# Optimization experiments

Measured on AMD Instinct MI355X. Metric: run time of the kernel, lower is better.

The kernel has to match this reference:

```python
import jax, jax.numpy as jnp
import numpy as np

B, C, D = 16384, 512, 512
EXT = 2
H = C * EXT
TAU = 1.0          # temperature_train
STEP = 0.05        # langevin_step_size
NOISE = 0.1        # langevin_noise
STEPS = 32         # langevin_steps


def setup_inputs() -> dict:
    key = jax.random.key(0)
    ks = jax.random.split(key, 8)
    s_in = 1.0 / np.sqrt(D)
    s_h = 1.0 / np.sqrt(H)
    return {
        'x': jax.random.normal(ks[0], (B, D), jnp.float32),
        'vanilla_components': jnp.abs(jax.random.normal(ks[1], (C, D), jnp.float32) * 0.1),
        'e_sp': jax.random.normal(ks[2], (C * D,), jnp.float32) * 0.1,
        'W1e': jax.random.normal(ks[3], (D, H), jnp.float32) * s_in,
        'b1e': jnp.zeros((H,), jnp.float32),
        'W2e': jax.random.normal(ks[4], (H, C), jnp.float32) * s_h,
        'b2e': jnp.zeros((C,), jnp.float32),
        'W1r': jax.random.normal(ks[5], (D, H), jnp.float32) * s_in,
        'b1r': jnp.zeros((H,), jnp.float32),
        'W2r': jax.random.normal(ks[6], (H, C), jnp.float32) * s_h,
        'b2r': jnp.zeros((C,), jnp.float32),
    }


def _langevin_gate(e, key):
    """Langevin MCMC on latent u with quadratic energy E(u)=0.5||u||^2 + <e,u>.
    Returns selection probability sigmoid(-u/tau)."""
    def step(u, k):
        grad = u + e  # dE/du
        u = u - STEP * grad + NOISE * jax.random.normal(k, u.shape, u.dtype)
        return u, None
    u, _ = jax.lax.scan(step, jnp.zeros_like(e), jax.random.split(key, STEPS))
    return jax.nn.sigmoid(-u / TAU)


def reference(x, vanilla_components, e_sp, W1e, b1e, W2e, b2e, W1r, b1r, W2r, b2r):
    k1, k2 = jax.random.split(jax.random.key(42))
    # non-negative components
    comps = jnp.abs(vanilla_components)  # [C, D]
    # fixed energy-based sparsity mask over component entries
    p_sp = _langevin_gate(e_sp, k1).reshape(C, D)
    comps = comps * p_sp
    # dynamic per-sample component selection energies via MLP
    h = jax.nn.relu(x @ W1e + b1e)          # [B, H]
    e_dyn = h @ W2e + b2e                   # [B, C]
    gate = _langevin_gate(e_dyn, k2)        # [B, C] soft gates (train mode)
    hr = jax.nn.relu(x @ W1r + b1r)         # [B, H]
    conc = (hr @ W2r + b2r) * gate          # [B, C]
    # aggregate: (concentration * components).sum over components -> [B, D]
    return conc @ comps
```

## Files before the change

### kernel.cpp

```cpp
#include <hip/hip_runtime.h>
#include <hip/hip_bf16.h>
#include <stdint.h>

#define Bn 16384
#define Cn 512
#define Dn 512
#define Hn 1024

#define A32 0.80628851f

typedef __attribute__((ext_vector_type(8))) short bf16x8;
typedef __attribute__((ext_vector_type(4))) float f32x4;
typedef __attribute__((ext_vector_type(2))) float f32x2;

__device__ __forceinline__ ushort f2bf(float f) {
  uint32_t u = __float_as_uint(f);
  return (ushort)((u + 0x7fffu + ((u >> 16) & 1u)) >> 16);
}
__device__ __forceinline__ float b2f(ushort u) {
  return __uint_as_float((uint32_t)u << 16);
}

typedef __attribute__((address_space(3))) uint32_t lds_u32_t;
typedef const __attribute__((address_space(1))) uint32_t glb_u32_t;
__device__ __forceinline__ void gload16(const ushort* g, ushort* l) {
  __builtin_amdgcn_global_load_lds((glb_u32_t*)g, (lds_u32_t*)l, 16, 0, 0);
}

constexpr uint32_t crotl(uint32_t v, int s) {
  return (v << s) | (v >> (32 - s));
}
struct TFOut { uint32_t w0, w1; };
constexpr TFOut ctf(uint32_t k0, uint32_t k1, uint32_t x0, uint32_t x1) {
  const uint32_t ks[3] = {k0, k1, k0 ^ k1 ^ 0x1BD11BDAu};
  const int rot[8] = {13, 15, 26, 6, 17, 29, 16, 24};
  uint32_t a = x0 + k0, b = x1 + k1;
  for (int g = 0; g < 5; ++g) {
    for (int i = 0; i < 4; ++i) {
      int r = rot[(g & 1) * 4 + i];
      a += b; b = crotl(b, r); b ^= a;
    }
    a += ks[(g + 1) % 3];
    b += ks[(g + 2) % 3] + (uint32_t)(g + 1);
  }
  return {a, b};
}
struct KeySched { uint32_t s[64]; uint32_t d[64]; };
constexpr KeySched make_keys() {
  KeySched K{};
  TFOut k1 = ctf(0u, 42u, 0u, 0u);
  TFOut k2 = ctf(0u, 42u, 0u, 1u);
  for (uint32_t t = 0; t < 32; ++t) {
    TFOut ws = ctf(k1.w0, k1.w1, 0u, t);
    K.s[2 * t] = ws.w0; K.s[2 * t + 1] = ws.w1;
    TFOut wd = ctf(k2.w0, k2.w1, 0u, t);
    K.d[2 * t] = wd.w0; K.d[2 * t + 1] = wd.w1;
  }
  return K;
}
__constant__ KeySched KS = make_keys();

__device__ __forceinline__ uint32_t rotl32(uint32_t v, int s) {
  return __builtin_rotateleft32(v, (uint32_t)s);
}
__device__ __forceinline__ uint32_t tf_xor(uint32_t K0, uint32_t K1,
                                           uint32_t KX, uint32_t j) {
  uint32_t a = K0, b = K1 + j;
#define TR(r) { a += b; b = rotl32(b, (r)); b ^= a; }
  TR(13) TR(15) TR(26) TR(6)   a += K1; b += KX + 1u;
  TR(17) TR(29) TR(16) TR(24)  a += KX; b += K0 + 2u;
  TR(13) TR(15) TR(26) TR(6)   a += K0; b += K1 + 3u;
  TR(17) TR(29) TR(16) TR(24)  a += K1; b += KX + 4u;
  TR(13) TR(15) TR(26) TR(6)   a += KX; b += K0 + 5u;
#undef TR
  return a ^ b;
}

__device__ __forceinline__ float bits_to_normal(uint32_t bits) {
  float f = __uint_as_float((bits >> 9) | 0x3f800000u) - 1.0f;
  float x = f * 2.0f - 0x1.fffffep-1f;
  float w = -__logf(1.0f - x * x);
  float p;
  if (w < 5.0f) {
    w -= 2.5f;
    p =            2.81022636e-08f;
    p = fmaf(p, w, 3.43273939e-07f);
    p = fmaf(p, w, -3.5233877e-06f);
    p = fmaf(p, w, -4.39150654e-06f);
    p = fmaf(p, w, 0.00021858087f);
    p = fmaf(p, w, -0.00125372503f);
    p = fmaf(p, w, -0.00417768164f);
    p = fmaf(p, w, 0.246640727f);
    p = fmaf(p, w, 1.50140941f);
  } else {
    w = sqrtf(w) - 3.0f;
    p =            -0.000200214257f;
    p = fmaf(p, w, 0.000100950558f);
    p = fmaf(p, w, 0.00134934322f);
    p = fmaf(p, w, -0.00367342844f);
    p = fmaf(p, w, 0.00573950773f);
    p = fmaf(p, w, -0.0076224613f);
    p = fmaf(p, w, 0.00943887047f);
    p = fmaf(p, w, 1.00167406f);
    p = fmaf(p, w, 2.83297682f);
  }
  return 0x1.6a09e6p+0f * (p * x);
}

__device__ __forceinline__ void z_block(ushort* __restrict__ Z, uint32_t zidx) {
  const uint32_t j0 = (zidx * 256u + threadIdx.x) * 2u;
  const uint32_t j1 = j0 + 1u;
  float z0 = 0.0f, z1 = 0.0f;
#pragma unroll 4
  for (int t = 0; t < 32; ++t) {
    const uint32_t K0 = KS.d[2 * t], K1 = KS.d[2 * t + 1];
    const uint32_t KX = K0 ^ K1 ^ 0x1BD11BDAu;
    uint32_t a0 = K0, b0 = K1 + j0;
    uint32_t a1 = K0, b1 = K1 + j1;
#define R2(r)                                                  \
    a0 += b0; a1 += b1;                                        \
    b0 = rotl32(b0, (r)); b1 = rotl32(b1, (r));                \
    b0 ^= a0; b1 ^= a1;
#define I2(p, q) a0 += (p); a1 += (p); b0 += (q); b1 += (q);
    R2(13) R2(15) R2(26) R2(6)  I2(K1, KX + 1u)
    R2(17) R2(29) R2(16) R2(24) I2(KX, K0 + 2u)
    R2(13) R2(15) R2(26) R2(6)  I2(K0, K1 + 3u)
    R2(17) R2(29) R2(16) R2(24) I2(K1, KX + 4u)
    R2(13) R2(15) R2(26) R2(6)  I2(KX, K0 + 5u)
#undef R2
#undef I2
    uint32_t s0 = a0 ^ b0, s1 = a1 ^ b1;
    float f0 = __uint_as_float((s0 >> 9) | 0x3f800000u) - 1.0f;
    float f1 = __uint_as_float((s1 >> 9) | 0x3f800000u) - 1.0f;
    float x0 = f0 * 2.0f - 0x1.fffffep-1f;
    float x1 = f1 * 2.0f - 0x1.fffffep-1f;
    float w0 = fminf(-__logf(fmaf(-x0, x0, 1.0f)), 5.0f) - 2.5f;
    float w1 = fminf(-__logf(fmaf(-x1, x1, 1.0f)), 5.0f) - 2.5f;
    f32x2 X = {x0, x1}, W = {w0, w1};
    f32x2 P = {2.81022636e-08f, 2.81022636e-08f};
    P = __builtin_elementwise_fma(P, W, (f32x2){3.43273939e-07f, 3.43273939e-07f});
    P = __builtin_elementwise_fma(P, W, (f32x2){-3.5233877e-06f, -3.5233877e-06f});
    P = __builtin_elementwise_fma(P, W, (f32x2){-4.39150654e-06f, -4.39150654e-06f});
    P = __builtin_elementwise_fma(P, W, (f32x2){0.00021858087f, 0.00021858087f});
    P = __builtin_elementwise_fma(P, W, (f32x2){-0.00125372503f, -0.00125372503f});
    P = __builtin_elementwise_fma(P, W, (f32x2){-0.00417768164f, -0.00417768164f});
    P = __builtin_elementwise_fma(P, W, (f32x2){0.246640727f, 0.246640727f});
    P = __builtin_elementwise_fma(P, W, (f32x2){1.50140941f, 1.50140941f});
    f32x2 Q = (P * X) * (f32x2){0.14142135f, 0.14142135f};
    z0 = fmaf(0.95f, z0, Q.x);
    z1 = fmaf(0.95f, z1, Q.y);
  }
  *(ushort2*)(Z + j0) = make_ushort2(f2bf(z0), f2bf(z1));
}

__device__ __forceinline__ void transpose_tile(
    const float* __restrict__ in, ushort* __restrict__ out,
    int N, int K, int tIdx, float T[32][33]) {
  const int ntn = N / 32;
  const int tk = tIdx / ntn, tn = tIdx % ntn;
  const int tx = threadIdx.x & 31, ty = threadIdx.x >> 5;
  const int k0 = tk * 32, n0 = tn * 32;
#pragma unroll
  for (int r = 0; r < 32; r += 8)
    T[ty + r][tx] = in[(size_t)(k0 + ty + r) * N + n0 + tx];
  __syncthreads();
#pragma unroll
  for (int r = 0; r < 32; r += 8)
    out[(size_t)(n0 + ty + r) * K + k0 + tx] = f2bf(T[tx][ty + r]);
}

__device__ __forceinline__ void smask_block(
    const float* __restrict__ vc, const float* __restrict__ e_sp,
    ushort* __restrict__ compsT, int g) {
  uint32_t jj = (uint32_t)g * 256 + threadIdx.x;
  uint32_t c = jj & (Cn - 1), d = jj >> 9;
  uint32_t ridx = c * Dn + d;
  float e = e_sp[ridx];
  float u = 0.0f;
#pragma unroll 4
  for (int t = 0; t < 32; ++t) {
    const uint32_t K0 = KS.s[2 * t], K1 = KS.s[2 * t + 1];
    uint32_t s = tf_xor(K0, K1, K0 ^ K1 ^ 0x1BD11BDAu, ridx);
    float n = bits_to_normal(s);
    u = (u - 0.05f * (u + e)) + 0.1f * n;
  }
  float gt = 1.0f / (1.0f + __expf(u));
  compsT[jj] = f2bf(fabsf(vc[ridx]) * gt);
}

__global__ __launch_bounds__(256) void k_prep_z(
    const float* __restrict__ x, ushort* __restrict__ x_bf,
    const float* __restrict__ W1e, ushort* __restrict__ W1eT,
    const float* __restrict__ W2e, ushort* __restrict__ W2eT,
    const float* __restrict__ W1r, ushort* __restrict__ W1rT,
    const float* __restrict__ W2r, ushort* __restrict__ W2rT,
    const float* __restrict__ vc, const float* __restrict__ e_sp,
    ushort* __restrict__ compsT, ushort* __restrict__ Zd) {
  __shared__ float T[32][33];
  const int pos = blockIdx.x;
  if ((pos % 5) == 4) {
    z_block(Zd, (uint32_t)(pos / 5));
    return;
  }
  const int p = (pos / 5) * 4 + (pos % 5);
  if (p < 8192) {
    int i = (p * 256 + threadIdx.x) * 4;
    float4 v = *(const float4*)(x + i);
    *(ushort4*)(x_bf + i) =
        make_ushort4(f2bf(v.x), f2bf(v.y), f2bf(v.z), f2bf(v.w));
  } else if (p < 8704) {
    transpose_tile(W1e, W1eT, Hn, Dn, p - 8192, T);
  } else if (p < 9216) {
    transpose_tile(W2e, W2eT, Cn, Hn, p - 8704, T);
  } else if (p < 9728) {
    transpose_tile(W1r, W1rT, Hn, Dn, p - 9216, T);
  } else if (p < 10240) {
    transpose_tile(W2r, W2rT, Cn, Hn, p - 9728, T);
  } else {
    smask_block(vc, e_sp, compsT, p - 10240);
  }
}

__device__ __forceinline__ void gemm_core(
    const ushort* __restrict__ A, const ushort* __restrict__ WT,
    int m0, int n0, int LD, int K,
    ushort* __restrict__ AsL, ushort* __restrict__ BsL,
    f32x4 acc[4][4]) {
  const int t = threadIdx.x;
  const int wave = t >> 6, lane = t & 63;
  const int row = t >> 2, col8 = (t & 3) << 3;
  const int wm = (wave >> 1) << 6, wn = (wave & 1) << 6;
  const int quad = lane >> 4, l15 = lane & 15;

  const ushort* ga0 = A  + (size_t)(m0 + row) * LD + col8;
  const ushort* ga1 = A  + (size_t)(m0 + 64 + row) * LD + col8;
  const ushort* gb0 = WT + (size_t)(n0 + row) * LD + col8;
  const ushort* gb1 = WT + (size_t)(n0 + 64 + row) * LD + col8;
  ushort* la0 = AsL + wave * 512;
  ushort* la1 = AsL + 2048 + wave * 512;
  ushort* lb0 = BsL + wave * 512;
  ushort* lb1 = BsL + 2048 + wave * 512;

  for (int k0 = 0; k0 < K; k0 += 32) {
    gload16(ga0 + k0, la0);
    gload16(ga1 + k0, la1);
    gload16(gb0 + k0, lb0);
    gload16(gb1 + k0, lb1);
    __syncthreads();
    bf16x8 af[4], bfr[4];
#pragma unroll
    for (int i = 0; i < 4; ++i) {
      af[i]  = *(const bf16x8*)&AsL[(wm + i * 16 + l15) * 32 + quad * 8];
      bfr[i] = *(const bf16x8*)&BsL[(wn + i * 16 + l15) * 32 + quad * 8];
    }
#pragma unroll
    for (int i = 0; i < 4; ++i)
#pragma unroll
      for (int j = 0; j < 4; ++j)
        acc[i][j] = __builtin_amdgcn_mfma_f32_16x16x32_bf16(af[i], bfr[j],
                                                            acc[i][j], 0, 0, 0);
    __syncthreads();
  }
}

__device__ __forceinline__ void gemm_tile_bf(
    const ushort* __restrict__ A, const ushort* __restrict__ WT,
    const float* __restrict__ bias, ushort* __restrict__ Out, int g,
    ushort* AsL, ushort* BsL) {
  const int n0 = (g & 7) * 128, m0 = (g >> 3) * 128;
  const int t = threadIdx.x;
  const int wave = t >> 6, lane = t & 63;
  const int wm = (wave >> 1) << 6, wn = (wave & 1) << 6;
  const int quad = lane >> 4, l15 = lane & 15;
  f32x4 acc[4][4] = {};
  gemm_core(A, WT, m0, n0, Dn, Dn, AsL, BsL, acc);
#pragma unroll
  for (int i = 0; i < 4; ++i)
#pragma unroll
    for (int j = 0; j < 4; ++j) {
      const int col = n0 + wn + j * 16 + l15;
      const float bv = bias[col];
#pragma unroll
      for (int r = 0; r < 4; ++r) {
        const int row = m0 + wm + i * 16 + quad * 4 + r;
        Out[(size_t)row * Hn + col] = f2bf(fmaxf(acc[i][j][r] + bv, 0.0f));
      }
    }
}

__global__ __launch_bounds__(256) void k_g13_z(
    const ushort* __restrict__ x_bf,
    const ushort* __restrict__ W1eT, const float* __restrict__ b1e,
    ushort* __restrict__ h,
    const ushort* __restrict__ W1rT, const float* __restrict__ b1r,
    ushort* __restrict__ hr, ushort* __restrict__ Zd) {
  __shared__ ushort AsL[4096];
  __shared__ ushort BsL[4096];
  const int pos = blockIdx.x;
  if (pos % 3) {
    z_block(Zd, 2816u + (uint32_t)(pos / 3) * 2u + (uint32_t)(pos % 3) - 1u);
    return;
  }
  const int gg = pos / 3;
  const int g = gg >> 1;
  if (gg & 1)
    gemm_tile_bf(x_bf, W1rT, b1r, hr, g, AsL, BsL);
  else
    gemm_tile_bf(x_bf, W1eT, b1e, h, g, AsL, BsL);
}

__device__ __forceinline__ void gemm_tile_f32out(
    const ushort* __restrict__ A, const ushort* __restrict__ WT,
    const float* __restrict__ bias, float* __restrict__ Out,
    int m0, int n0, ushort* AsL, ushort* BsL) {
  const int t = threadIdx.x;
  const int wave = t >> 6, lane = t & 63;
  const int wm = (wave >> 1) << 6, wn = (wave & 1) << 6;
  const int quad = lane >> 4, l15 = lane & 15;
  f32x4 acc[4][4] = {};
  gemm_core(A, WT, m0, n0, Hn, Hn, AsL, BsL, acc);
#pragma unroll
  for (int i = 0; i < 4; ++i)
#pragma unroll
    for (int j = 0; j < 4; ++j) {
      const int col = n0 + wn + j * 16 + l15;
      const float bv = bias[col];
#pragma unroll
      for (int r = 0; r < 4; ++r) {
        const int row = m0 + wm + i * 16 + quad * 4 + r;
        Out[(size_t)row * Cn + col] = acc[i][j][r] + bv;
      }
    }
}

__global__ __launch_bounds__(256) void k_e_z(
    const ushort* __restrict__ h, const ushort* __restrict__ W2eT,
    const float* __restrict__ b2e, float* __restrict__ e_out,
    ushort* __restrict__ Zd) {
  __shared__ ushort AsL[4096];
  __shared__ ushort BsL[4096];
  const int pos = blockIdx.x;
  if ((pos % 10) == 0) {
    const int tg = pos / 10;
    gemm_tile_f32out(h, W2eT, b2e, e_out, (tg >> 2) * 128, (tg & 3) * 128,
                     AsL, BsL);
  } else {
    z_block(Zd, 6912u + (uint32_t)(pos / 10) * 9u + (uint32_t)(pos % 10) - 1u);
  }
}

__global__ __launch_bounds__(256) void k_r_z(
    const ushort* __restrict__ hr, const ushort* __restrict__ W2rT,
    const float* __restrict__ b2r, float* __restrict__ cr_out,
    ushort* __restrict__ Zd) {
  __shared__ ushort AsL[4096];
  __shared__ ushort BsL[4096];
  const int pos = blockIdx.x;
  if (pos >= 5120) {
    z_block(Zd, 16128u + (uint32_t)(pos - 5120));
    return;
  }
  if ((pos % 10) == 0) {
    const int tg = pos / 10;
    gemm_tile_f32out(hr, W2rT, b2r, cr_out, (tg >> 2) * 128, (tg & 3) * 128,
                     AsL, BsL);
  } else {
    z_block(Zd, 11520u + (uint32_t)(pos / 10) * 9u + (uint32_t)(pos % 10) - 1u);
  }
}

__global__ __launch_bounds__(256) void k_gate(
    const float* __restrict__ e, const float* __restrict__ cr,
    ushort* __restrict__ Z) {
  const size_t i = ((size_t)blockIdx.x * 256u + threadIdx.x) * 8u;
  uint4 zv = *(const uint4*)(Z + i);
  ushort zs[8];
  *(uint4*)zs = zv;
  float ee[8], cc[8];
  *(float4*)(ee)     = *(const float4*)(e + i);
  *(float4*)(ee + 4) = *(const float4*)(e + i + 4);
  *(float4*)(cc)     = *(const float4*)(cr + i);
  *(float4*)(cc + 4) = *(const float4*)(cr + i + 4);
  ushort os[8];
#pragma unroll
  for (int k = 0; k < 8; ++k) {
    float z = b2f(zs[k]);
    float g = 1.0f / (1.0f + __expf(z - A32 * ee[k]));
    os[k] = f2bf(cc[k] * g);
  }
  *(uint4*)(Z + i) = *(uint4*)os;
}

__global__ __launch_bounds__(256) void k_gemm_out(
    const ushort* __restrict__ A, const ushort* __restrict__ WT,
    float* __restrict__ Out) {
  __shared__ ushort AsL[4096];
  __shared__ ushort BsL[4096];
  const int t = threadIdx.x;
  const int m0 = blockIdx.y * 128, n0 = blockIdx.x * 128;
  const int wave = t >> 6, lane = t & 63;
  const int wm = (wave >> 1) << 6, wn = (wave & 1) << 6;
  const int quad = lane >> 4, l15 = lane & 15;
  f32x4 acc[4][4] = {};
  gemm_core(A, WT, m0, n0, Cn, Cn, AsL, BsL, acc);
#pragma unroll
  for (int i = 0; i < 4; ++i)
#pragma unroll
    for (int j = 0; j < 4; ++j) {
      const int col = n0 + wn + j * 16 + l15;
#pragma unroll
      for (int r = 0; r < 4; ++r) {
        const int row = m0 + wm + i * 16 + quad * 4 + r;
        Out[(size_t)row * Dn + col] = acc[i][j][r];
      }
    }
}

extern "C" void kernel_launch(void* const* d_in, const int* in_sizes, int n_in,
                              void* d_out, int out_size, void* d_ws, size_t ws_size,
                              hipStream_t stream) {
  const float* x    = (const float*)d_in[0];
  const float* vc   = (const float*)d_in[1];
  const float* e_sp = (const float*)d_in[2];
  const float* W1e  = (const float*)d_in[3];
  const float* b1e  = (const float*)d_in[4];
  const float* W2e  = (const float*)d_in[5];
  const float* b2e  = (const float*)d_in[6];
  const float* W1r  = (const float*)d_in[7];
  const float* b1r  = (const float*)d_in[8];
  const float* W2r  = (const float*)d_in[9];
  const float* b2r  = (const float*)d_in[10];
  float* out = (float*)d_out;

  char* ws = (char*)d_ws;
  ushort* W1eT   = (ushort*)(ws + (1u << 12));
  ushort* W2eT   = (ushort*)(ws + (1u << 12) + (1u << 20));
  ushort* W1rT   = (ushort*)(ws + (1u << 12) + (2u << 20));
  ushort* W2rT   = (ushort*)(ws + (1u << 12) + (3u << 20));
  ushort* compsT = (ushort*)(ws + (1u << 12) + (4u << 20));
  ushort* Zdyn   = (ushort*)(ws + (8u << 20));
  ushort* h_bf   = (ushort*)(ws + (24u << 20));
  ushort* hr_bf  = (ushort*)(ws + (56u << 20));
  float*  cr_f32 = (float*)(ws + (24u << 20));
  ushort* x_bf   = (ushort*)d_out;
  float*  e_f32  = (float*)d_out;

  k_prep_z<<<14080, 256, 0, stream>>>(x, x_bf, W1e, W1eT, W2e, W2eT,
                                      W1r, W1rT, W2r, W2rT, vc, e_sp, compsT,
                                      Zdyn);
  k_g13_z<<<6144, 256, 0, stream>>>(x_bf, W1eT, b1e, h_bf, W1rT, b1r, hr_bf,
                                    Zdyn);
  k_e_z<<<5120, 256, 0, stream>>>(h_bf, W2eT, b2e, e_f32, Zdyn);
  k_r_z<<<5376, 256, 0, stream>>>(hr_bf, W2rT, b2r, cr_f32, Zdyn);
  k_gate<<<4096, 256, 0, stream>>>(e_f32, cr_f32, Zdyn);
  k_gemm_out<<<dim3(Dn / 128, Bn / 128), 256, 0, stream>>>(Zdyn, compsT, out);
}
```

Before: 776.7 us.

## Swizzle LDS GEMM tiles and rebalance GEMM/noise block interleaving

Applies an XOR swizzle to the LDS column offset for A and B tiles, on both the write and the read side, to cut bank conflicts on the bf16x8 fragment loads. The fragment loop now loads B once and A one row at a time, which lowers register pressure. The three fused kernels change how GEMM tiles and noise-generation blocks are interleaved. GEMM tiles are now spread densely at the front of the grid, with the leftover z blocks placed at the end, so the long GEMM blocks get scheduled early. The risk is mis-indexed z_block ranges or a swizzle that does not match between store and load.

```diff
diff --git a/kernel.cpp b/kernel.cpp
--- a/kernel.cpp
+++ b/kernel.cpp
@@ -228,9 +228,11 @@
     f32x4 acc[4][4]) {
   const int t = threadIdx.x;
   const int wave = t >> 6, lane = t & 63;
-  const int row = t >> 2, col8 = (t & 3) << 3;
+  const int row = t >> 2;
+  const int col8 = ((t & 3) << 3) ^ ((((t >> 3)) & 3) << 3);
   const int wm = (wave >> 1) << 6, wn = (wave & 1) << 6;
   const int quad = lane >> 4, l15 = lane & 15;
+  const int rc = (quad << 3) ^ (((l15 >> 1) & 3) << 3);
 
   const ushort* ga0 = A  + (size_t)(m0 + row) * LD + col8;
   const ushort* ga1 = A  + (size_t)(m0 + 64 + row) * LD + col8;
@@ -247,18 +249,18 @@
     gload16(gb0 + k0, lb0);
     gload16(gb1 + k0, lb1);
     __syncthreads();
-    bf16x8 af[4], bfr[4];
+    bf16x8 bfr[4];
+#pragma unroll
+    for (int j = 0; j < 4; ++j)
+      bfr[j] = *(const bf16x8*)&BsL[(wn + j * 16 + l15) * 32 + rc];
 #pragma unroll
     for (int i = 0; i < 4; ++i) {
-      af[i]  = *(const bf16x8*)&AsL[(wm + i * 16 + l15) * 32 + quad * 8];
-      bfr[i] = *(const bf16x8*)&BsL[(wn + i * 16 + l15) * 32 + quad * 8];
-    }
-#pragma unroll
-    for (int i = 0; i < 4; ++i)
+      bf16x8 afi = *(const bf16x8*)&AsL[(wm + i * 16 + l15) * 32 + rc];
 #pragma unroll
       for (int j = 0; j < 4; ++j)
-        acc[i][j] = __builtin_amdgcn_mfma_f32_16x16x32_bf16(af[i], bfr[j],
+        acc[i][j] = __builtin_amdgcn_mfma_f32_16x16x32_bf16(afi, bfr[j],
                                                             acc[i][j], 0, 0, 0);
+    }
     __syncthreads();
   }
 }
@@ -297,11 +299,15 @@
   __shared__ ushort AsL[4096];
   __shared__ ushort BsL[4096];
   const int pos = blockIdx.x;
-  if (pos % 3) {
-    z_block(Zd, 2816u + (uint32_t)(pos / 3) * 2u + (uint32_t)(pos % 3) - 1u);
+  if (pos >= 4096) {
+    z_block(Zd, 2816u + 2048u + (uint32_t)(pos - 4096));
     return;
   }
-  const int gg = pos / 3;
+  if (pos & 1) {
+    z_block(Zd, 2816u + (uint32_t)(pos >> 1));
+    return;
+  }
+  const int gg = pos >> 1;
   const int g = gg >> 1;
   if (gg & 1)
     gemm_tile_bf(x_bf, W1rT, b1r, hr, g, AsL, BsL);
@@ -340,12 +346,16 @@
   __shared__ ushort AsL[4096];
   __shared__ ushort BsL[4096];
   const int pos = blockIdx.x;
-  if ((pos % 10) == 0) {
-    const int tg = pos / 10;
-    gemm_tile_f32out(h, W2eT, b2e, e_out, (tg >> 2) * 128, (tg & 3) * 128,
-                     AsL, BsL);
+  if (pos < 2048) {
+    if ((pos & 3) == 0) {
+      const int tg = pos >> 2;
+      gemm_tile_f32out(h, W2eT, b2e, e_out, (tg >> 2) * 128, (tg & 3) * 128,
+                       AsL, BsL);
+    } else {
+      z_block(Zd, 6912u + (uint32_t)(pos - 1 - (pos >> 2)));
+    }
   } else {
-    z_block(Zd, 6912u + (uint32_t)(pos / 10) * 9u + (uint32_t)(pos % 10) - 1u);
+    z_block(Zd, 6912u + (uint32_t)(pos - 512));
   }
 }
 
@@ -356,16 +366,16 @@
   __shared__ ushort AsL[4096];
   __shared__ ushort BsL[4096];
   const int pos = blockIdx.x;
-  if (pos >= 5120) {
-    z_block(Zd, 16128u + (uint32_t)(pos - 5120));
-    return;
-  }
-  if ((pos % 10) == 0) {
-    const int tg = pos / 10;
-    gemm_tile_f32out(hr, W2rT, b2r, cr_out, (tg >> 2) * 128, (tg & 3) * 128,
-                     AsL, BsL);
+  if (pos < 2048) {
+    if ((pos & 3) == 0) {
+      const int tg = pos >> 2;
+      gemm_tile_f32out(hr, W2rT, b2r, cr_out, (tg >> 2) * 128, (tg & 3) * 128,
+                       AsL, BsL);
+    } else {
+      z_block(Zd, 11520u + (uint32_t)(pos - 1 - (pos >> 2)));
+    }
   } else {
-    z_block(Zd, 11520u + (uint32_t)(pos / 10) * 9u + (uint32_t)(pos % 10) - 1u);
+    z_block(Zd, 11520u + (uint32_t)(pos - 512));
   }
 }
 
```

Measured after the change: 820.0 us. 1.06x slower.
